# Performance work log

Hardware: AMD Instinct MI355X
Metric: run time of the kernel (lower is better)

## Reference

```python
import jax, jax.numpy as jnp
import numpy as np

HEADS = 8
DIM_KEY = 256
NUM_KEYS = 256           # sqrt(num_experts)
PK_TOPK = 16             # product_key_topk (defaults to num_experts_per_head)
K_PER_HEAD = 16          # num_experts_per_head


def setup_inputs() -> dict:
    key = jax.random.key(0)
    k1, k2, k3, k4, k5 = jax.random.split(key, 5)
    b, n, d = 2, 1024, 512          # batch MUST be 2 (see module quirk)
    num_experts = NUM_KEYS * NUM_KEYS
    x = jax.random.normal(k1, (b, n, d), jnp.float32)
    Wq = jax.random.normal(k2, (2 * HEADS * DIM_KEY, d), jnp.float32) * 0.02
    keys = jax.random.normal(k3, (HEADS, NUM_KEYS, 2, DIM_KEY), jnp.float32)
    w_down = jax.random.normal(k4, (num_experts, d), jnp.float32) * 0.02
    w_up = jax.random.normal(k5, (num_experts, d), jnp.float32) * 0.02
    return {"x": x, "Wq": Wq, "keys": keys, "w_down": w_down, "w_up": w_up}


def reference(x, Wq, keys, w_down, w_up):
    b, n, d = x.shape  # b == 2 required by the original module's einsum/unpack
    # to_queries: Linear -> Unflatten(-1,(2,h,dk)) -> permute(0,2,1,3,4)
    q = (x @ Wq.T).reshape(b, n, 2, HEADS, DIM_KEY).transpose(0, 2, 1, 3, 4)  # (b,2,n,h,dk)
    kk = keys.transpose(2, 0, 1, 3)  # (2, h, num_keys, dk)
    # faithful to original: 'p' axis of queries is the BATCH axis (requires b==2)
    sim = jnp.einsum('pbnhd,phkd->pbnhk', q, kk)  # (2, 2, n, h, num_keys)
    sx, ix = jax.lax.top_k(sim[0], PK_TOPK)
    sy, iy = jax.lax.top_k(sim[1], PK_TOPK)
    # combine product keys: (2, n, h, T, T) -> (2, n, h, T*T)
    all_scores = (sx[..., :, None] + sy[..., None, :]).reshape(*sx.shape[:-1], PK_TOPK * PK_TOPK)
    all_indices = (ix[..., :, None] * NUM_KEYS + iy[..., None, :]).reshape(*ix.shape[:-1], PK_TOPK * PK_TOPK)
    scores, pk = jax.lax.top_k(all_scores, K_PER_HEAD)          # (2, n, h, K)
    indices = jnp.take_along_axis(all_indices, pk, axis=-1)     # (2, n, h, K)
    wd = w_down[indices]  # (2, n, h, K, d) huge gather
    wu = w_up[indices]    # (2, n, h, K, d)
    h = jnp.einsum('bnd,bnhkd->bnhk', x, wd)
    h = jax.nn.gelu(h, approximate=False)  # torch nn.GELU default = exact erf
    h = h * jax.nn.softmax(scores, axis=-1)
    return jnp.einsum('bnhk,bnhkd->bnd', h, wu)
```

## Files before the change

### kernel.cpp

```cpp
#include <hip/hip_runtime.h>
#include <hip/hip_bf16.h>
#include <math.h>

typedef __attribute__((ext_vector_type(8))) short bf16x8;
typedef __attribute__((ext_vector_type(4))) float f32x4;

__device__ __forceinline__ unsigned f2u(float f) {
    unsigned b = __float_as_uint(f);
    return b ^ ((unsigned)((int)b >> 31) | 0x80000000u);
}
__device__ __forceinline__ float u2f(unsigned u) {
    unsigned b = (u & 0x80000000u) ? (u ^ 0x80000000u) : ~u;
    return __uint_as_float(b);
}
__device__ __forceinline__ unsigned short f2bf(float f) {
    unsigned b = __float_as_uint(f);
    return (unsigned short)((b + 0x7FFFu + ((b >> 16) & 1u)) >> 16);
}
__device__ __forceinline__ float bflo(unsigned u) { return __uint_as_float(u << 16); }
__device__ __forceinline__ float bfhi(unsigned u) { return __uint_as_float(u & 0xFFFF0000u); }

__device__ __forceinline__ void radix16(unsigned u0, unsigned u1, unsigned u2, unsigned u3,
                                        unsigned& T, int& kk) {
    unsigned prefix = 0; int k = 16;
    for (int b = 31; b >= 0; --b) {
        unsigned hi = (prefix >> b) | 1u;
        int cnt = __popcll(__ballot((u0 >> b) == hi))
                + __popcll(__ballot((u1 >> b) == hi))
                + __popcll(__ballot((u2 >> b) == hi))
                + __popcll(__ballot((u3 >> b) == hi));
        if (cnt >= k) prefix |= (1u << b); else k -= cnt;
    }
    T = prefix; kk = k;
}

__global__ __launch_bounds__(256) void k_conv(const float* __restrict__ src,
                                              unsigned short* __restrict__ dst, int n8) {
    int tid = blockIdx.x * 256 + threadIdx.x;
    int stride = gridDim.x * 256;
    for (int i = tid; i < n8; i += stride) {
        float4 a = *(const float4*)&src[(size_t)i * 8];
        float4 b = *(const float4*)&src[(size_t)i * 8 + 4];
        uint4 o;
        o.x = (unsigned)f2bf(a.x) | ((unsigned)f2bf(a.y) << 16);
        o.y = (unsigned)f2bf(a.z) | ((unsigned)f2bf(a.w) << 16);
        o.z = (unsigned)f2bf(b.x) | ((unsigned)f2bf(b.y) << 16);
        o.w = (unsigned)f2bf(b.z) | ((unsigned)f2bf(b.w) << 16);
        *(uint4*)&dst[(size_t)i * 8] = o;
    }
}

__global__ __launch_bounds__(256) void kK2(const float* __restrict__ keys,
                                           const float* __restrict__ Wq,
                                           unsigned short* __restrict__ K2b) {
    __shared__ float As[16][128];
    __shared__ float Bs[16][128];
    int t  = threadIdx.x;
    int tx = t & 15, ty = t >> 4;
    int p = blockIdx.z;
    int ktile = blockIdx.y & 1, ch = blockIdx.y >> 1;
    int h = ch & 7, c = ch >> 3;
    int m0 = ktile * 128;
    int n0 = blockIdx.x * 128;
    const float* kb = keys + ((size_t)(h * 256 + m0) * 2 + p) * 256;
    const float* wb = Wq + (size_t)(c * 2048 + h * 256) * 512;
    float acc[8][8] = {};
    for (int k0 = 0; k0 < 256; k0 += 16) {
#pragma unroll
        for (int i = 0; i < 2; ++i) {
            int u   = t * 2 + i;
            int row = u >> 2;
            int kc  = (u & 3) << 2;
            float4 av = *(const float4*)&kb[(size_t)row * 512 + k0 + kc];
            As[kc + 0][row] = av.x; As[kc + 1][row] = av.y; As[kc + 2][row] = av.z; As[kc + 3][row] = av.w;
            int v = u;
            int dkrow = v >> 5;
            int dcol  = (v & 31) << 2;
            float4 bv = *(const float4*)&wb[(size_t)(k0 + dkrow) * 512 + n0 + dcol];
            *(float4*)&Bs[dkrow][dcol] = bv;
        }
        __syncthreads();
#pragma unroll
        for (int kk = 0; kk < 16; ++kk) {
            float4 a0 = *(const float4*)&As[kk][ty * 8];
            float4 a1 = *(const float4*)&As[kk][ty * 8 + 4];
            float4 b0 = *(const float4*)&Bs[kk][tx * 4];
            float4 b1 = *(const float4*)&Bs[kk][tx * 4 + 64];
            float a[8] = {a0.x, a0.y, a0.z, a0.w, a1.x, a1.y, a1.z, a1.w};
            float b[8] = {b0.x, b0.y, b0.z, b0.w, b1.x, b1.y, b1.z, b1.w};
#pragma unroll
            for (int i = 0; i < 8; ++i)
#pragma unroll
                for (int j = 0; j < 8; ++j) acc[i][j] += a[i] * b[j];
        }
        __syncthreads();
    }
    unsigned short* Cp = K2b + (size_t)p * 4096 * 512;
#pragma unroll
    for (int i = 0; i < 8; ++i) {
        int r = c * 2048 + h * 256 + m0 + ty * 8 + i;
        uint2 o0, o1;
        o0.x = (unsigned)f2bf(acc[i][0]) | ((unsigned)f2bf(acc[i][1]) << 16);
        o0.y = (unsigned)f2bf(acc[i][2]) | ((unsigned)f2bf(acc[i][3]) << 16);
        o1.x = (unsigned)f2bf(acc[i][4]) | ((unsigned)f2bf(acc[i][5]) << 16);
        o1.y = (unsigned)f2bf(acc[i][6]) | ((unsigned)f2bf(acc[i][7]) << 16);
        *(uint2*)&Cp[(size_t)r * 512 + n0 + tx * 4]      = o0;
        *(uint2*)&Cp[(size_t)r * 512 + n0 + 64 + tx * 4] = o1;
    }
}

__global__ __launch_bounds__(256) void kS_mfma(const unsigned short* __restrict__ xb,
                                               const unsigned short* __restrict__ k2b,
                                               float* __restrict__ S) {
    int t = threadIdx.x;
    int wv = t >> 6, ln = t & 63;
    int p  = blockIdx.z;
    int n0 = blockIdx.y * 128 + wv * 32;
    int e0 = blockIdx.x * 64;
    const unsigned short* A = xb  + (size_t)p * 1024 * 512;
    const unsigned short* B = k2b + (size_t)p * 4096 * 512;
    int lr = ln & 15;
    int lk = (ln >> 4) * 8;

    f32x4 acc00 = {}, acc01 = {}, acc02 = {}, acc03 = {};
    f32x4 acc10 = {}, acc11 = {}, acc12 = {}, acc13 = {};

    for (int k0 = 0; k0 < 512; k0 += 32) {
        bf16x8 a0 = *(const bf16x8*)&A[(size_t)(n0 + lr) * 512 + k0 + lk];
        bf16x8 a1 = *(const bf16x8*)&A[(size_t)(n0 + 16 + lr) * 512 + k0 + lk];
        bf16x8 b0 = *(const bf16x8*)&B[(size_t)(e0 + lr) * 512 + k0 + lk];
        bf16x8 b1 = *(const bf16x8*)&B[(size_t)(e0 + 16 + lr) * 512 + k0 + lk];
        bf16x8 b2 = *(const bf16x8*)&B[(size_t)(e0 + 32 + lr) * 512 + k0 + lk];
        bf16x8 b3 = *(const bf16x8*)&B[(size_t)(e0 + 48 + lr) * 512 + k0 + lk];
        acc00 = __builtin_amdgcn_mfma_f32_16x16x32_bf16(a0, b0, acc00, 0, 0, 0);
        acc01 = __builtin_amdgcn_mfma_f32_16x16x32_bf16(a0, b1, acc01, 0, 0, 0);
        acc02 = __builtin_amdgcn_mfma_f32_16x16x32_bf16(a0, b2, acc02, 0, 0, 0);
        acc03 = __builtin_amdgcn_mfma_f32_16x16x32_bf16(a0, b3, acc03, 0, 0, 0);
        acc10 = __builtin_amdgcn_mfma_f32_16x16x32_bf16(a1, b0, acc10, 0, 0, 0);
        acc11 = __builtin_amdgcn_mfma_f32_16x16x32_bf16(a1, b1, acc11, 0, 0, 0);
        acc12 = __builtin_amdgcn_mfma_f32_16x16x32_bf16(a1, b2, acc12, 0, 0, 0);
        acc13 = __builtin_amdgcn_mfma_f32_16x16x32_bf16(a1, b3, acc13, 0, 0, 0);
    }

    float* C = S + (size_t)p * 1024 * 4096;
    int rbase = (ln >> 4) * 4;
    int cw = ln & 15;
#define STORE_FRAG(ACC, AF, BF)                                                   \
    {                                                                             \
        _Pragma("unroll")                                                         \
        for (int r = 0; r < 4; ++r)                                               \
            C[(size_t)(n0 + (AF)*16 + rbase + r) * 4096 + e0 + (BF)*16 + cw] = ACC[r]; \
    }
    STORE_FRAG(acc00, 0, 0); STORE_FRAG(acc01, 0, 1); STORE_FRAG(acc02, 0, 2); STORE_FRAG(acc03, 0, 3);
    STORE_FRAG(acc10, 1, 0); STORE_FRAG(acc11, 1, 1); STORE_FRAG(acc12, 1, 2); STORE_FRAG(acc13, 1, 3);
#undef STORE_FRAG
}

__global__ __launch_bounds__(256) void k2_topk(const float* __restrict__ S,
                                               int* __restrict__ widx,
                                               float* __restrict__ wcoef) {
    __shared__ float sx_s[4][2][16];
    __shared__ int   ix_s[4][2][16];

    int t = threadIdx.x;
    int wv = t >> 6, ln = t & 63;
    int task = blockIdx.x * 4 + wv;
    int c = task >> 13;
    int n = (task >> 3) & 1023;
    int h = task & 7;
    unsigned long long lt = (1ull << ln) - 1ull;

    const float* s0p = S + (size_t)n * 4096 + c * 2048 + h * 256 + ln * 4;
    float4 s0 = *(const float4*)&s0p[0];
    float4 s1 = *(const float4*)&s0p[1024UL * 4096];

#define TK_HALF(PIDX, V)                                                          \
    {                                                                             \
        unsigned u0 = f2u(V.x), u1 = f2u(V.y), u2 = f2u(V.z), u3 = f2u(V.w);      \
        unsigned T; int kk;                                                       \
        radix16(u0, u1, u2, u3, T, kk);                                           \
        int base = 0;                                                             \
        { unsigned long long m = __ballot(u0 > T);                                \
          if (u0 > T) { int pos = base + __popcll(m & lt);                        \
              sx_s[wv][PIDX][pos] = V.x; ix_s[wv][PIDX][pos] = ln * 4 + 0; }      \
          base += __popcll(m); }                                                  \
        { unsigned long long m = __ballot(u1 > T);                                \
          if (u1 > T) { int pos = base + __popcll(m & lt);                        \
              sx_s[wv][PIDX][pos] = V.y; ix_s[wv][PIDX][pos] = ln * 4 + 1; }      \
          base += __popcll(m); }                                                  \
        { unsigned long long m = __ballot(u2 > T);                                \
          if (u2 > T) { int pos = base + __popcll(m & lt);                        \
              sx_s[wv][PIDX][pos] = V.z; ix_s[wv][PIDX][pos] = ln * 4 + 2; }      \
          base += __popcll(m); }                                                  \
        { unsigned long long m = __ballot(u3 > T);                                \
          if (u3 > T) { int pos = base + __popcll(m & lt);                        \
              sx_s[wv][PIDX][pos] = V.w; ix_s[wv][PIDX][pos] = ln * 4 + 3; }      \
          base += __popcll(m); }                                                  \
        { unsigned long long m = __ballot(u0 == T); int r = __popcll(m & lt);     \
          if ((u0 == T) && r < kk) { sx_s[wv][PIDX][base + r] = V.x;              \
              ix_s[wv][PIDX][base + r] = ln * 4 + 0; }                            \
          int cn2 = __popcll(m); int tk = cn2 < kk ? cn2 : kk; base += tk; kk -= tk; } \
        { unsigned long long m = __ballot(u1 == T); int r = __popcll(m & lt);     \
          if ((u1 == T) && r < kk) { sx_s[wv][PIDX][base + r] = V.y;              \
              ix_s[wv][PIDX][base + r] = ln * 4 + 1; }                            \
          int cn2 = __popcll(m); int tk = cn2 < kk ? cn2 : kk; base += tk; kk -= tk; } \
        { unsigned long long m = __ballot(u2 == T); int r = __popcll(m & lt);     \
          if ((u2 == T) && r < kk) { sx_s[wv][PIDX][base + r] = V.z;              \
              ix_s[wv][PIDX][base + r] = ln * 4 + 2; }                            \
          int cn2 = __popcll(m); int tk = cn2 < kk ? cn2 : kk; base += tk; kk -= tk; } \
        { unsigned long long m = __ballot(u3 == T); int r = __popcll(m & lt);     \
          if ((u3 == T) && r < kk) { sx_s[wv][PIDX][base + r] = V.w;              \
              ix_s[wv][PIDX][base + r] = ln * 4 + 3; }                            \
          int cn2 = __popcll(m); int tk = cn2 < kk ? cn2 : kk; base += tk; kk -= tk; } \
    }
    TK_HALF(0, s0);
    TK_HALF(1, s1);
#undef TK_HALF
    __syncthreads();

    int t0 = ln, t1 = ln + 64, t2 = ln + 128, t3 = ln + 192;
    float vc0 = sx_s[wv][0][t0 >> 4] + sx_s[wv][1][t0 & 15];
    float vc1 = sx_s[wv][0][t1 >> 4] + sx_s[wv][1][t1 & 15];
    float vc2 = sx_s[wv][0][t2 >> 4] + sx_s[wv][1][t2 & 15];
    float vc3 = sx_s[wv][0][t3 >> 4] + sx_s[wv][1][t3 & 15];
    unsigned u0 = f2u(vc0), u1 = f2u(vc1), u2 = f2u(vc2), u3 = f2u(vc3);
    unsigned T; int kk;
    radix16(u0, u1, u2, u3, T, kk);
    float Tf = u2f(T);

    bool w0 = u0 > T, w1 = u1 > T, w2 = u2 > T, w3 = u3 > T;
    int q0 = 0, q1 = 0, q2 = 0, q3 = 0;
    int base = 0;
    { unsigned long long m = __ballot(w0); q0 = base + __popcll(m & lt); base += __popcll(m); }
    { unsigned long long m = __ballot(w1); q1 = base + __popcll(m & lt); base += __popcll(m); }
    { unsigned long long m = __ballot(w2); q2 = base + __popcll(m & lt); base += __popcll(m); }
    { unsigned long long m = __ballot(w3); q3 = base + __popcll(m & lt); base += __popcll(m); }
#define CMB_EQ(UJ, WJ, QJ) { unsigned long long m = __ballot(UJ == T);          \
    int r = __popcll(m & lt);                                                   \
    if ((UJ == T) && r < kk) { WJ = true; QJ = base + r; }                      \
    int cn2 = __popcll(m); int tk = cn2 < kk ? cn2 : kk;                        \
    base += tk; kk -= tk; }
    CMB_EQ(u0, w0, q0); CMB_EQ(u1, w1, q1); CMB_EQ(u2, w2, q2); CMB_EQ(u3, w3, q3);
#undef CMB_EQ

    float e0 = 0.f, e1 = 0.f, e2 = 0.f, e3 = 0.f;
    int id0 = 0, id1 = 0, id2 = 0, id3 = 0;
    float es = 0.f;
    if (w0) { e0 = __expf(vc0 - Tf); es += e0; id0 = ix_s[wv][0][t0 >> 4] * 256 + ix_s[wv][1][t0 & 15]; }
    if (w1) { e1 = __expf(vc1 - Tf); es += e1; id1 = ix_s[wv][0][t1 >> 4] * 256 + ix_s[wv][1][t1 & 15]; }
    if (w2) { e2 = __expf(vc2 - Tf); es += e2; id2 = ix_s[wv][0][t2 >> 4] * 256 + ix_s[wv][1][t2 & 15]; }
    if (w3) { e3 = __expf(vc3 - Tf); es += e3; id3 = ix_s[wv][0][t3 >> 4] * 256 + ix_s[wv][1][t3 & 15]; }
    for (int s = 1; s < 64; s <<= 1) es += __shfl_xor(es, s);
    float inv = 1.f / es;

    int off = ((c * 1024 + n) * 8 + h) * 16;
    if (w0) { wcoef[off + q0] = e0 * inv; widx[off + q0] = id0; }
    if (w1) { wcoef[off + q1] = e1 * inv; widx[off + q1] = id1; }
    if (w2) { wcoef[off + q2] = e2 * inv; widx[off + q2] = id2; }
    if (w3) { wcoef[off + q3] = e3 * inv; widx[off + q3] = id3; }
}

__global__ __launch_bounds__(256) void k3_experts_bf16(const float* __restrict__ x,
                                                       const unsigned short* __restrict__ wd,
                                                       const unsigned short* __restrict__ wu,
                                                       const int* __restrict__ widx,
                                                       const float* __restrict__ wcoef,
                                                       float* __restrict__ out) {
    int bid = blockIdx.x;
    int c = bid >> 10, n = bid & 1023;
    int t = threadIdx.x, wv = t >> 6, ln = t & 63;
    __shared__ float wacc[4][512];

    const float* xrow = &x[(c * 1024 + n) * 512];
    float xr[8], oacc[8];
    {
        float4 xa = *(const float4*)&xrow[ln * 8];
        float4 xb = *(const float4*)&xrow[ln * 8 + 4];
        xr[0] = xa.x; xr[1] = xa.y; xr[2] = xa.z; xr[3] = xa.w;
        xr[4] = xb.x; xr[5] = xb.y; xr[6] = xb.z; xr[7] = xb.w;
    }
#pragma unroll
    for (int j = 0; j < 8; ++j) oacc[j] = 0.f;

    const int base = (c * 1024 + n) * 128;
    for (int e = wv * 32; e < wv * 32 + 32; ++e) {
        int   idx = widx[base + e];
        float wgt = wcoef[base + e];
        uint4 dv = *(const uint4*)&wd[(size_t)idx * 512 + ln * 8];
        float part = bflo(dv.x) * xr[0] + bfhi(dv.x) * xr[1]
                   + bflo(dv.y) * xr[2] + bfhi(dv.y) * xr[3]
                   + bflo(dv.z) * xr[4] + bfhi(dv.z) * xr[5]
                   + bflo(dv.w) * xr[6] + bfhi(dv.w) * xr[7];
        for (int s = 1; s < 64; s <<= 1) part += __shfl_xor(part, s);
        float hv = part;
        float coef = 0.5f * hv * (1.f + erff(hv * 0.70710678118654752f)) * wgt;
        uint4 uv = *(const uint4*)&wu[(size_t)idx * 512 + ln * 8];
        oacc[0] += coef * bflo(uv.x); oacc[1] += coef * bfhi(uv.x);
        oacc[2] += coef * bflo(uv.y); oacc[3] += coef * bfhi(uv.y);
        oacc[4] += coef * bflo(uv.z); oacc[5] += coef * bfhi(uv.z);
        oacc[6] += coef * bflo(uv.w); oacc[7] += coef * bfhi(uv.w);
    }

#pragma unroll
    for (int j = 0; j < 8; ++j) wacc[wv][ln * 8 + j] = oacc[j];
    __syncthreads();

    float* orow = &out[(c * 1024 + n) * 512];
    for (int d = t; d < 512; d += 256)
        orow[d] = wacc[0][d] + wacc[1][d] + wacc[2][d] + wacc[3][d];
}

__global__ __launch_bounds__(256) void k3_experts_f32(const float* __restrict__ x,
                                                      const float* __restrict__ w_down,
                                                      const float* __restrict__ w_up,
                                                      const int* __restrict__ widx,
                                                      const float* __restrict__ wcoef,
                                                      float* __restrict__ out) {
    int bid = blockIdx.x;
    int c = bid >> 10, n = bid & 1023;
    int t = threadIdx.x, wv = t >> 6, ln = t & 63;
    __shared__ float wacc[4][512];

    const float* xrow = &x[(c * 1024 + n) * 512];
    float xr[8], oacc[8];
    {
        float4 xa = *(const float4*)&xrow[ln * 8];
        float4 xb = *(const float4*)&xrow[ln * 8 + 4];
        xr[0] = xa.x; xr[1] = xa.y; xr[2] = xa.z; xr[3] = xa.w;
        xr[4] = xb.x; xr[5] = xb.y; xr[6] = xb.z; xr[7] = xb.w;
    }
#pragma unroll
    for (int j = 0; j < 8; ++j) oacc[j] = 0.f;

    const int base = (c * 1024 + n) * 128;
    for (int e = wv * 32; e < wv * 32 + 32; ++e) {
        int   idx = widx[base + e];
        float wgt = wcoef[base + e];
        const float* dr = &w_down[(long)idx * 512 + ln * 8];
        float4 da = *(const float4*)&dr[0];
        float4 db = *(const float4*)&dr[4];
        float part = da.x * xr[0] + da.y * xr[1] + da.z * xr[2] + da.w * xr[3]
                   + db.x * xr[4] + db.y * xr[5] + db.z * xr[6] + db.w * xr[7];
        for (int s = 1; s < 64; s <<= 1) part += __shfl_xor(part, s);
        float hv = part;
        float coef = 0.5f * hv * (1.f + erff(hv * 0.70710678118654752f)) * wgt;
        const float* ur = &w_up[(long)idx * 512 + ln * 8];
        float4 ua = *(const float4*)&ur[0];
        float4 ub = *(const float4*)&ur[4];
        oacc[0] += coef * ua.x; oacc[1] += coef * ua.y; oacc[2] += coef * ua.z; oacc[3] += coef * ua.w;
        oacc[4] += coef * ub.x; oacc[5] += coef * ub.y; oacc[6] += coef * ub.z; oacc[7] += coef * ub.w;
    }
#pragma unroll
    for (int j = 0; j < 8; ++j) wacc[wv][ln * 8 + j] = oacc[j];
    __syncthreads();

    float* orow = &out[(c * 1024 + n) * 512];
    for (int d = t; d < 512; d += 256)
        orow[d] = wacc[0][d] + wacc[1][d] + wacc[2][d] + wacc[3][d];
}

extern "C" void kernel_launch(void* const* d_in, const int* in_sizes, int n_in,
                              void* d_out, int out_size, void* d_ws, size_t ws_size,
                              hipStream_t stream) {
    const float* x      = (const float*)d_in[0];
    const float* Wq     = (const float*)d_in[1];
    const float* keys   = (const float*)d_in[2];
    const float* w_down = (const float*)d_in[3];
    const float* w_up   = (const float*)d_in[4];
    float* out = (float*)d_out;

    char* ws = (char*)d_ws;
    size_t off = 0;
    float* S     = (float*)(ws + off); off += 2048UL * 4096 * 4;
    int*   widx  = (int*)(ws + off);   off += 262144UL * 4;
    float* wcoef = (float*)(ws + off); off += 262144UL * 4;
    unsigned short* K2b = (unsigned short*)(ws + off); off += 2UL * 4096 * 512 * 2;
    unsigned short* xb  = (unsigned short*)(ws + off); off += 2048UL * 512 * 2;
    unsigned short* wd16 = (unsigned short*)(ws + off); off += 65536UL * 512 * 2;
    unsigned short* wu16 = (unsigned short*)(ws + off); off += 65536UL * 512 * 2;
    bool use_bf16 = (ws_size >= off);

    k_conv<<<512, 256, 0, stream>>>(x, xb, 2048 * 512 / 8);
    kK2<<<dim3(4, 32, 2), 256, 0, stream>>>(keys, Wq, K2b);
    kS_mfma<<<dim3(64, 8, 2), 256, 0, stream>>>(xb, K2b, S);
    k2_topk<<<4096, 256, 0, stream>>>(S, widx, wcoef);
    if (use_bf16) {
        k_conv<<<2048, 256, 0, stream>>>(w_down, wd16, 65536 * 512 / 8);
        k_conv<<<2048, 256, 0, stream>>>(w_up,   wu16, 65536 * 512 / 8);
        k3_experts_bf16<<<2048, 256, 0, stream>>>(x, wd16, wu16, widx, wcoef, out);
    } else {
        k3_experts_f32<<<2048, 256, 0, stream>>>(x, w_down, w_up, widx, wcoef, out);
    }
}
```

Measured before the change: 294.4 us.

## Interleave bf16 down/up expert rows and fuse their conversion into one kernel

The two bf16 conversion kernels for w_down and w_up are replaced by a single kernel that writes both into one interleaved buffer, with each expert's down row followed by its up row. The expert kernel then loads the down and up vectors together from one contiguous 2 KB row before the reduction, so the up-row fetch is issued early and overlaps the shuffle reduction. This aims to cut a kernel launch and improve gather locality and latency hiding. It costs a few more live registers in the expert loop, and the workspace size is unchanged.

```diff
diff --git a/kernel.cpp b/kernel.cpp
--- a/kernel.cpp
+++ b/kernel.cpp
@@ -47,6 +47,38 @@
         o.z = (unsigned)f2bf(b.x) | ((unsigned)f2bf(b.y) << 16);
         o.w = (unsigned)f2bf(b.z) | ((unsigned)f2bf(b.w) << 16);
         *(uint4*)&dst[(size_t)i * 8] = o;
+    }
+}
+
+__global__ __launch_bounds__(256) void k_convi(const float* __restrict__ wd,
+                                               const float* __restrict__ wu,
+                                               unsigned short* __restrict__ wdu) {
+    int gid = blockIdx.x * 256 + threadIdx.x;
+    int wave = gid >> 6, ln = gid & 63;
+    int nw = (gridDim.x * 256) >> 6;
+    for (int e = wave; e < 65536; e += nw) {
+        {
+            const float* s = wd + (size_t)e * 512 + ln * 8;
+            float4 a = *(const float4*)&s[0];
+            float4 b = *(const float4*)&s[4];
+            uint4 o;
+            o.x = (unsigned)f2bf(a.x) | ((unsigned)f2bf(a.y) << 16);
+            o.y = (unsigned)f2bf(a.z) | ((unsigned)f2bf(a.w) << 16);
+            o.z = (unsigned)f2bf(b.x) | ((unsigned)f2bf(b.y) << 16);
+            o.w = (unsigned)f2bf(b.z) | ((unsigned)f2bf(b.w) << 16);
+            *(uint4*)&wdu[(size_t)e * 1024 + ln * 8] = o;
+        }
+        {
+            const float* s = wu + (size_t)e * 512 + ln * 8;
+            float4 a = *(const float4*)&s[0];
+            float4 b = *(const float4*)&s[4];
+            uint4 o;
+            o.x = (unsigned)f2bf(a.x) | ((unsigned)f2bf(a.y) << 16);
+            o.y = (unsigned)f2bf(a.z) | ((unsigned)f2bf(a.w) << 16);
+            o.z = (unsigned)f2bf(b.x) | ((unsigned)f2bf(b.y) << 16);
+            o.w = (unsigned)f2bf(b.z) | ((unsigned)f2bf(b.w) << 16);
+            *(uint4*)&wdu[(size_t)e * 1024 + 512 + ln * 8] = o;
+        }
     }
 }
 
@@ -261,8 +293,7 @@
 }
 
 __global__ __launch_bounds__(256) void k3_experts_bf16(const float* __restrict__ x,
-                                                       const unsigned short* __restrict__ wd,
-                                                       const unsigned short* __restrict__ wu,
+                                                       const unsigned short* __restrict__ wdu,
                                                        const int* __restrict__ widx,
                                                        const float* __restrict__ wcoef,
                                                        float* __restrict__ out) {
@@ -286,7 +317,9 @@
     for (int e = wv * 32; e < wv * 32 + 32; ++e) {
         int   idx = widx[base + e];
         float wgt = wcoef[base + e];
-        uint4 dv = *(const uint4*)&wd[(size_t)idx * 512 + ln * 8];
+        const unsigned short* row = wdu + (size_t)idx * 1024;
+        uint4 dv = *(const uint4*)&row[ln * 8];
+        uint4 uv = *(const uint4*)&row[512 + ln * 8];
         float part = bflo(dv.x) * xr[0] + bfhi(dv.x) * xr[1]
                    + bflo(dv.y) * xr[2] + bfhi(dv.y) * xr[3]
                    + bflo(dv.z) * xr[4] + bfhi(dv.z) * xr[5]
@@ -294,7 +327,6 @@
         for (int s = 1; s < 64; s <<= 1) part += __shfl_xor(part, s);
         float hv = part;
         float coef = 0.5f * hv * (1.f + erff(hv * 0.70710678118654752f)) * wgt;
-        uint4 uv = *(const uint4*)&wu[(size_t)idx * 512 + ln * 8];
         oacc[0] += coef * bflo(uv.x); oacc[1] += coef * bfhi(uv.x);
         oacc[2] += coef * bflo(uv.y); oacc[3] += coef * bfhi(uv.y);
         oacc[4] += coef * bflo(uv.z); oacc[5] += coef * bfhi(uv.z);
@@ -376,8 +408,7 @@
     float* wcoef = (float*)(ws + off); off += 262144UL * 4;
     unsigned short* K2b = (unsigned short*)(ws + off); off += 2UL * 4096 * 512 * 2;
     unsigned short* xb  = (unsigned short*)(ws + off); off += 2048UL * 512 * 2;
-    unsigned short* wd16 = (unsigned short*)(ws + off); off += 65536UL * 512 * 2;
-    unsigned short* wu16 = (unsigned short*)(ws + off); off += 65536UL * 512 * 2;
+    unsigned short* wdu = (unsigned short*)(ws + off); off += 65536UL * 1024 * 2;
     bool use_bf16 = (ws_size >= off);
 
     k_conv<<<512, 256, 0, stream>>>(x, xb, 2048 * 512 / 8);
@@ -385,9 +416,8 @@
     kS_mfma<<<dim3(64, 8, 2), 256, 0, stream>>>(xb, K2b, S);
     k2_topk<<<4096, 256, 0, stream>>>(S, widx, wcoef);
     if (use_bf16) {
-        k_conv<<<2048, 256, 0, stream>>>(w_down, wd16, 65536 * 512 / 8);
-        k_conv<<<2048, 256, 0, stream>>>(w_up,   wu16, 65536 * 512 / 8);
-        k3_experts_bf16<<<2048, 256, 0, stream>>>(x, wd16, wu16, widx, wcoef, out);
+        k_convi<<<2048, 256, 0, stream>>>(w_down, w_up, wdu);
+        k3_experts_bf16<<<2048, 256, 0, stream>>>(x, wdu, widx, wcoef, out);
     } else {
         k3_experts_f32<<<2048, 256, 0, stream>>>(x, w_down, w_up, widx, wcoef, out);
     }
```

Measured after the change: 293.7 us. About the same (-0.2%).
